# Performance work log

Measured on AMD Instinct MI355X. Metric: run time of the kernel, lower is better.

The kernel has to match this reference:

```python
import jax, jax.numpy as jnp
import numpy as np

B, C_IN, C_OUT, N, K = 4, 64, 64, 100000, 6
EPS = 1e-5  # BatchNorm2d default eps


def setup_inputs() -> dict:
    key = jax.random.key(0)
    k1, k2, k3, k4 = jax.random.split(key, 4)
    x = jax.random.normal(k1, (B, C_IN, N), jnp.float32)
    neigh = jax.random.randint(k2, (B, N, K), 0, N, jnp.int32)
    # bias-free 1x2 conv weights (center feature + neighbor-sum symmetric operator)
    W0 = jax.random.normal(k3, (C_OUT, C_IN, 2), jnp.float32) * (1.0 / np.sqrt(C_IN * 2))
    W1 = jax.random.normal(k4, (C_OUT, C_OUT, 2), jnp.float32) * (1.0 / np.sqrt(C_OUT * 2))
    gamma = jnp.ones((C_OUT,), jnp.float32)
    beta = jnp.zeros((C_OUT,), jnp.float32)
    return {"x": x, "neigh": neigh, "W0": W0, "W1": W1, "gamma": gamma, "beta": beta}


def _mesh_conv_point(x, neigh, W):
    # x: [B, C, N], neigh: [B, N, K] -> gather neighbor features [B, C, N, K]
    nb = jax.vmap(lambda xb, ib: xb[:, ib])(x, neigh)
    # symmetric operator stack: center feature and sum over neighbors -> [B, C, N, 2]
    G = jnp.stack([x, nb.sum(axis=-1)], axis=-1)
    # 1x2 conv (bias=False) as einsum -> [B, O, N]
    return jnp.einsum('bcns,ocs->bon', G, W)


def _batchnorm(h, gamma, beta):
    # training-mode batch stats over (batch, vertex) per channel
    mean = h.mean(axis=(0, 2), keepdims=True)
    var = h.var(axis=(0, 2), keepdims=True)
    return (h - mean) * jax.lax.rsqrt(var + EPS) * gamma[None, :, None] + beta[None, :, None]


def reference(x, neigh, W0, W1, gamma, beta):
    h = _mesh_conv_point(x, neigh, W0)
    x1 = h  # residual branch
    h = _batchnorm(jax.nn.relu(h), gamma, beta)
    h = _mesh_conv_point(h, neigh, W1)
    h = h + x1
    return jax.nn.relu(h)
```

## Files before the change

kernel.cpp:

```cpp
#include <hip/hip_runtime.h>
#include <hip/hip_bf16.h>

#define BB   4
#define NN   100000
#define TOT  (BB * NN)
#define KK   6
#define EPSV 1e-5f

using bf16   = __hip_bfloat16;
using ushort = unsigned short;
typedef __attribute__((ext_vector_type(8))) short  short8;
typedef __attribute__((ext_vector_type(4))) float  float4v;

union U4S8 { uint4 u; short8 s; };

__device__ __forceinline__ unsigned f2bu(float f) {
    union { bf16 h; ushort u; } c; c.h = __float2bfloat16(f); return c.u;
}
__device__ __forceinline__ unsigned pk(float a, float b) {
    return f2bu(a) | (f2bu(b) << 16);
}
__device__ __forceinline__ float blo(unsigned x) {
    union { unsigned u; float f; } c; c.u = x << 16; return c.f;
}
__device__ __forceinline__ float bhi(unsigned x) {
    union { unsigned u; float f; } c; c.u = x & 0xFFFF0000u; return c.f;
}
__device__ __forceinline__ unsigned relu2(unsigned x) {
    unsigned lo = (unsigned)(((int)(x << 16)) >> 31) & 0x0000FFFFu;
    unsigned hi = ((unsigned)(((int)x) >> 31)) << 16;
    return x & ~(lo | hi);
}
__device__ __forceinline__ int batch_base(int g) {
    return (g >= 3 * NN) ? 3 * NN : (g >= 2 * NN) ? 2 * NN : (g >= NN) ? NN : 0;
}

__global__ void wprep0_k(const float* __restrict__ W0, ushort* __restrict__ Wf0)
{
    int L = blockIdx.x * 256 + threadIdx.x;
    if (L < 8192) {
        int i = L & 7, lane = (L >> 3) & 63, r = L >> 9;
        int s = r & 1, t = r >> 1;
        int o = (t & 3) * 16 + (lane & 15);
        int c = s * 32 + (lane >> 4) * 8 + i;
        Wf0[L] = f2bu(W0[o * 128 + c * 2 + (t >> 2)]);
    }
}

__global__ __launch_bounds__(256) void xpose_k(const float* __restrict__ x,
                                               ushort* __restrict__ xT)
{
    __shared__ float tile[64][65];
    const int b  = blockIdx.y;
    const int n0 = blockIdx.x * 64;
    const int tx = threadIdx.x & 63;
    const int ty = threadIdx.x >> 6;
    const float* xb = x + (size_t)b * 64 * NN;
    const int n = n0 + tx;
#pragma unroll
    for (int cc = 0; cc < 64; cc += 4) {
        const int c = cc + ty;
        tile[tx][c] = (n < NN) ? xb[(size_t)c * NN + n] : 0.f;
    }
    __syncthreads();
#pragma unroll
    for (int rr = 0; rr < 64; rr += 4) {
        const int nl = rr + ty;
        const int n2 = n0 + nl;
        if (n2 < NN) xT[((size_t)b * NN + n2) * 64 + tx] = (ushort)f2bu(tile[nl][tx]);
    }
}

__global__ __launch_bounds__(256, 3) void gemm1_k(
    const ushort* __restrict__ xT, const ushort* __restrict__ Wf,
    ushort* __restrict__ Uu, ushort* __restrict__ Uv)
{
    const int wave = threadIdx.x >> 6;
    const int lane = threadIdx.x & 63;
    const int col  = lane & 15;
    const int quad = lane >> 4;

    short8 wf[8][2];
#pragma unroll
    for (int t = 0; t < 8; ++t)
#pragma unroll
        for (int s = 0; s < 2; ++s)
            wf[t][s] = *(const short8*)(Wf + ((t * 2 + s) * 64 + lane) * 8);

    const int wid = blockIdx.x * 4 + wave;
    for (int tile = wid; tile < 25000; tile += 2500) {
        const size_t g0 = (size_t)tile * 16;
        const ushort* ar = xT + (g0 + col) * 64 + quad * 8;
        short8 p0 = *(const short8*)(ar);
        short8 p1 = *(const short8*)(ar + 32);

        float4v acc[8];
#pragma unroll
        for (int t = 0; t < 8; ++t) acc[t] = (float4v){0.f, 0.f, 0.f, 0.f};
#pragma unroll
        for (int t = 0; t < 8; ++t)
            acc[t] = __builtin_amdgcn_mfma_f32_16x16x32_bf16(wf[t][0], p0, acc[t], 0, 0, 0);
#pragma unroll
        for (int t = 0; t < 8; ++t)
            acc[t] = __builtin_amdgcn_mfma_f32_16x16x32_bf16(wf[t][1], p1, acc[t], 0, 0, 0);

#pragma unroll
        for (int t = 0; t < 8; ++t) {
            uint2 d;
            d.x = pk(acc[t][0], acc[t][1]);
            d.y = pk(acc[t][2], acc[t][3]);
            ushort* base = (t < 4) ? Uu : Uv;
            *(uint2*)(base + (g0 + col) * 64 + (t & 3) * 16 + quad * 4) = d;
        }
    }
}

__global__ __launch_bounds__(256, 4) void gather1_k(
    const ushort* __restrict__ Uu, const ushort* __restrict__ Uv,
    const int* __restrict__ neigh, ushort* __restrict__ hT,
    float* __restrict__ stats)
{
    __shared__ float red[4][128];
    const int wave = threadIdx.x >> 6;
    const int lane = threadIdx.x & 63;
    const int q    = lane >> 4;
    const int cpos = lane & 15;
    const int g0   = (blockIdx.x * 4 + wave) * 64;

    float sA[4] = {0, 0, 0, 0}, sB[4] = {0, 0, 0, 0};

    for (int it = 0; it < 8; ++it) {
        const int gb = g0 + it * 8;
        int gp[2], gc[2], bo[2];
        gp[0] = gb + q;     gp[1] = gb + 4 + q;
        gc[0] = (gp[0] < TOT) ? gp[0] : (TOT - 1);
        gc[1] = (gp[1] < TOT) ? gp[1] : (TOT - 1);
        bo[0] = batch_base(gc[0]);
        bo[1] = batch_base(gc[1]);

        int idx[2][6];
#pragma unroll
        for (int i = 0; i < 2; ++i)
#pragma unroll
            for (int k = 0; k < 6; ++k)
                idx[i][k] = neigh[(size_t)gc[i] * 6 + k];

        uint2 uu[2], vv[2][6];
#pragma unroll
        for (int i = 0; i < 2; ++i)
            uu[i] = *(const uint2*)(Uu + (size_t)gc[i] * 64 + cpos * 4);
#pragma unroll
        for (int i = 0; i < 2; ++i)
#pragma unroll
            for (int k = 0; k < 6; ++k)
                vv[i][k] = *(const uint2*)(Uv + (size_t)(bo[i] + idx[i][k]) * 64 + cpos * 4);

#pragma unroll
        for (int i = 0; i < 2; ++i) {
            float h[4];
            h[0] = blo(uu[i].x); h[1] = bhi(uu[i].x);
            h[2] = blo(uu[i].y); h[3] = bhi(uu[i].y);
#pragma unroll
            for (int k = 0; k < 6; ++k) {
                h[0] += blo(vv[i][k].x); h[1] += bhi(vv[i][k].x);
                h[2] += blo(vv[i][k].y); h[3] += bhi(vv[i][k].y);
            }
            if (gp[i] < TOT) {
                uint2 st;
                st.x = pk(h[0], h[1]);
                st.y = pk(h[2], h[3]);
                *(uint2*)(hT + (size_t)gp[i] * 64 + cpos * 4) = st;
#pragma unroll
                for (int j = 0; j < 4; ++j) {
                    float rv = fmaxf(h[j], 0.f);
                    sA[j] += rv;
                    sB[j]  = fmaf(rv, rv, sB[j]);
                }
            }
        }
    }

#pragma unroll
    for (int d = 16; d < 64; d <<= 1)
#pragma unroll
        for (int j = 0; j < 4; ++j) {
            sA[j] += __shfl_xor(sA[j], d);
            sB[j] += __shfl_xor(sB[j], d);
        }
    if (q == 0) {
#pragma unroll
        for (int j = 0; j < 4; ++j) {
            red[wave][cpos * 4 + j]      = sA[j];
            red[wave][64 + cpos * 4 + j] = sB[j];
        }
    }
    __syncthreads();
    if (threadIdx.x < 128) {
        float v = red[0][threadIdx.x] + red[1][threadIdx.x]
                + red[2][threadIdx.x] + red[3][threadIdx.x];
        atomicAdd(&stats[threadIdx.x], v);
    }
}

__global__ void bnA_k(const float* __restrict__ stats, const float* __restrict__ gamma,
                      const float* __restrict__ beta, float* __restrict__ ab)
{
    const int o = threadIdx.x;
    if (o < 64) {
        const float inv = 1.f / (float)TOT;
        float mean = stats[o] * inv;
        float var  = stats[64 + o] * inv - mean * mean;
        float a    = gamma[o] * rsqrtf(var + EPSV);
        ab[o]      = a;
        ab[64 + o] = fmaf(-a, mean, beta[o]);
    }
}

__global__ __launch_bounds__(256) void bnB_k(
    const float* __restrict__ ab, const float* __restrict__ W1,
    ushort* __restrict__ Wf1, float* __restrict__ bias)
{
    if (blockIdx.x < 32) {
        int L = blockIdx.x * 256 + threadIdx.x;
        int i = L & 7, lane = (L >> 3) & 63, r = L >> 9;
        int s = r & 1, t = r >> 1;
        int o = (t & 3) * 16 + (lane & 15);
        int c = s * 32 + (lane >> 4) * 8 + i;
        Wf1[L] = f2bu(ab[c] * W1[o * 128 + c * 2 + (t >> 2)]);
    } else if (threadIdx.x < 128) {
        const int part = threadIdx.x >> 6, o = threadIdx.x & 63;
        float s = 0.f;
#pragma unroll
        for (int c = 0; c < 64; ++c)
            s = fmaf(ab[64 + c], W1[o * 128 + c * 2 + part], s);
        bias[threadIdx.x] = s;
    }
}

__global__ __launch_bounds__(256, 3) void gemm2_k(
    const ushort* __restrict__ hT, const ushort* __restrict__ Wf,
    const float* __restrict__ bias, ushort* __restrict__ Up,
    ushort* __restrict__ Uq)
{
    const int wave = threadIdx.x >> 6;
    const int lane = threadIdx.x & 63;
    const int col  = lane & 15;
    const int quad = lane >> 4;

    short8 wf[8][2];
#pragma unroll
    for (int t = 0; t < 8; ++t)
#pragma unroll
        for (int s = 0; s < 2; ++s)
            wf[t][s] = *(const short8*)(Wf + ((t * 2 + s) * 64 + lane) * 8);

    float4v binit[8];
#pragma unroll
    for (int t = 0; t < 8; ++t)
#pragma unroll
        for (int r = 0; r < 4; ++r)
            binit[t][r] = bias[t * 16 + quad * 4 + r];

    const int wid = blockIdx.x * 4 + wave;
    for (int tile = wid; tile < 25000; tile += 2500) {
        const size_t g0 = (size_t)tile * 16;
        const ushort* ar = hT + (g0 + col) * 64 + quad * 8;
        U4S8 p0, p1;
        p0.u = *(const uint4*)(ar);
        p1.u = *(const uint4*)(ar + 32);
        p0.u.x = relu2(p0.u.x); p0.u.y = relu2(p0.u.y);
        p0.u.z = relu2(p0.u.z); p0.u.w = relu2(p0.u.w);
        p1.u.x = relu2(p1.u.x); p1.u.y = relu2(p1.u.y);
        p1.u.z = relu2(p1.u.z); p1.u.w = relu2(p1.u.w);

        float4v acc[8];
#pragma unroll
        for (int t = 0; t < 8; ++t) acc[t] = binit[t];
#pragma unroll
        for (int t = 0; t < 8; ++t)
            acc[t] = __builtin_amdgcn_mfma_f32_16x16x32_bf16(wf[t][0], p0.s, acc[t], 0, 0, 0);
#pragma unroll
        for (int t = 0; t < 8; ++t)
            acc[t] = __builtin_amdgcn_mfma_f32_16x16x32_bf16(wf[t][1], p1.s, acc[t], 0, 0, 0);

#pragma unroll
        for (int t = 0; t < 8; ++t) {
            uint2 d;
            d.x = pk(acc[t][0], acc[t][1]);
            d.y = pk(acc[t][2], acc[t][3]);
            ushort* base = (t < 4) ? Up : Uq;
            *(uint2*)(base + (g0 + col) * 64 + (t & 3) * 16 + quad * 4) = d;
        }
    }
}

__global__ __launch_bounds__(256, 4) void gather2_k(
    const ushort* __restrict__ Up, const ushort* __restrict__ Uq,
    const ushort* __restrict__ hT, const int* __restrict__ neigh,
    float* __restrict__ out)
{
    __shared__ float ts[64][65];
    const int wave = threadIdx.x >> 6;
    const int lane = threadIdx.x & 63;
    const int q    = lane >> 4;
    const int cpos = lane & 15;
    const int g0   = blockIdx.x * 64;

#pragma unroll
    for (int it = 0; it < 2; ++it) {
        const int gb = g0 + wave * 16 + it * 8;
        int gp[2], bo[2];
        gp[0] = gb + q;  gp[1] = gb + 4 + q;
        bo[0] = batch_base(gp[0]);
        bo[1] = batch_base(gp[1]);

        int idx[2][6];
#pragma unroll
        for (int i = 0; i < 2; ++i)
#pragma unroll
            for (int k = 0; k < 6; ++k)
                idx[i][k] = neigh[(size_t)gp[i] * 6 + k];

        uint2 pp[2], rr[2], qq[2][6];
#pragma unroll
        for (int i = 0; i < 2; ++i) {
            pp[i] = *(const uint2*)(Up + (size_t)gp[i] * 64 + cpos * 4);
            rr[i] = *(const uint2*)(hT + (size_t)gp[i] * 64 + cpos * 4);
        }
#pragma unroll
        for (int i = 0; i < 2; ++i)
#pragma unroll
            for (int k = 0; k < 6; ++k)
                qq[i][k] = *(const uint2*)(Uq + (size_t)(bo[i] + idx[i][k]) * 64 + cpos * 4);

#pragma unroll
        for (int i = 0; i < 2; ++i) {
            float h[4];
            h[0] = blo(pp[i].x) + blo(rr[i].x); h[1] = bhi(pp[i].x) + bhi(rr[i].x);
            h[2] = blo(pp[i].y) + blo(rr[i].y); h[3] = bhi(pp[i].y) + bhi(rr[i].y);
#pragma unroll
            for (int k = 0; k < 6; ++k) {
                h[0] += blo(qq[i][k].x); h[1] += bhi(qq[i][k].x);
                h[2] += blo(qq[i][k].y); h[3] += bhi(qq[i][k].y);
            }
            const int pl = wave * 16 + it * 8 + i * 4 + q;
#pragma unroll
            for (int j = 0; j < 4; ++j)
                ts[cpos * 4 + j][pl] = fmaxf(h[j], 0.f);
        }
    }
    __syncthreads();

    const int g2  = g0 + lane;
    const int bo2 = batch_base(g2);
    const int b2  = (g2 >= 3 * NN) ? 3 : (g2 >= 2 * NN) ? 2 : (g2 >= NN) ? 1 : 0;
    const int n2  = g2 - bo2;
#pragma unroll
    for (int r = 0; r < 16; ++r) {
        const int o = wave * 16 + r;
        out[((size_t)b2 * 64 + o) * NN + n2] = ts[o][lane];
    }
}

extern "C" void kernel_launch(void* const* d_in, const int* in_sizes, int n_in,
                              void* d_out, int out_size, void* d_ws, size_t ws_size,
                              hipStream_t stream)
{
    const float* x     = (const float*)d_in[0];
    const int*   neigh = (const int*)d_in[1];
    const float* W0    = (const float*)d_in[2];
    const float* W1    = (const float*)d_in[3];
    const float* gamma = (const float*)d_in[4];
    const float* beta  = (const float*)d_in[5];
    float* out = (float*)d_out;

    char* ws = (char*)d_ws;
    ushort* xT    = (ushort*)(ws + 0);
    ushort* hT    = (ushort*)(ws + 0);
    ushort* Uu    = (ushort*)(ws + 51200000);
    ushort* Uv    = (ushort*)(ws + 102400000);
    ushort* Up    = Uu;
    ushort* Uq    = Uv;
    float*  stats = (float*)(ws + 153600000);
    float*  ab    = (float*)(ws + 153600512);
    ushort* Wf0   = (ushort*)(ws + 153601024);
    ushort* Wf1   = (ushort*)(ws + 153617408);
    float*  bias  = (float*)(ws + 153633792);

    hipMemsetAsync(stats, 0, 512, stream);
    wprep0_k<<<dim3(32), dim3(256), 0, stream>>>(W0, Wf0);
    xpose_k<<<dim3((NN + 63) / 64, BB), dim3(256), 0, stream>>>(x, xT);
    gemm1_k<<<dim3(625), dim3(256), 0, stream>>>(xT, Wf0, Uu, Uv);
    gather1_k<<<dim3(1563), dim3(256), 0, stream>>>(Uu, Uv, neigh, hT, stats);
    bnA_k<<<dim3(1), dim3(64), 0, stream>>>(stats, gamma, beta, ab);
    bnB_k<<<dim3(33), dim3(256), 0, stream>>>(ab, W1, Wf1, bias);
    gemm2_k<<<dim3(625), dim3(256), 0, stream>>>(hT, Wf1, bias, Up, Uq);
    gather2_k<<<dim3(TOT / 64), dim3(256), 0, stream>>>(Up, Uq, hT, neigh, out);
}
```

Measured before the change: 432.5 us.

## Stage neighbor gathers through LDS via global_load_lds with swizzled rows

Both gather kernels now fetch the six neighbor rows with 16-byte global_load_lds direct-to-LDS loads into a per-wave staging buffer, using a rotating swizzle so the LDS reads avoid bank conflicts. Each lane handles 8 channels with 16-byte loads and stores instead of 4 channels with 8-byte accesses, and neighbor indices are read as uint2 pairs. gather1 is relaunched with twice the blocks and fewer points per wave. The aim is wider, fewer memory transactions and less register pressure from in-flight gathers. In exchange it adds LDS use, lowers the occupancy hint to 3, and waits on vmcnt(0) every iteration, so loads from one iteration cannot overlap the next.

```diff
diff --git a/kernel.cpp b/kernel.cpp
--- a/kernel.cpp
+++ b/kernel.cpp
@@ -33,6 +33,13 @@
 }
 __device__ __forceinline__ int batch_base(int g) {
     return (g >= 3 * NN) ? 3 * NN : (g >= 2 * NN) ? 2 * NN : (g >= NN) ? NN : 0;
+}
+
+__device__ __forceinline__ void gload_lds16(const void* g, void* l)
+{
+    __builtin_amdgcn_global_load_lds(
+        (const __attribute__((address_space(1))) unsigned int*)g,
+        (__attribute__((address_space(3))) unsigned int*)l, 16, 0, 0);
 }
 
 __global__ void wprep0_k(const float* __restrict__ W0, ushort* __restrict__ Wf0)
@@ -115,83 +122,77 @@
     }
 }
 
-__global__ __launch_bounds__(256, 4) void gather1_k(
+__global__ __launch_bounds__(256, 3) void gather1_k(
     const ushort* __restrict__ Uu, const ushort* __restrict__ Uv,
     const int* __restrict__ neigh, ushort* __restrict__ hT,
     float* __restrict__ stats)
 {
+    __shared__ __align__(1024) ushort stage[4][3072];
     __shared__ float red[4][128];
     const int wave = threadIdx.x >> 6;
     const int lane = threadIdx.x & 63;
-    const int q    = lane >> 4;
-    const int cpos = lane & 15;
-    const int g0   = (blockIdx.x * 4 + wave) * 64;
-
-    float sA[4] = {0, 0, 0, 0}, sB[4] = {0, 0, 0, 0};
-
-    for (int it = 0; it < 8; ++it) {
-        const int gb = g0 + it * 8;
-        int gp[2], gc[2], bo[2];
-        gp[0] = gb + q;     gp[1] = gb + 4 + q;
-        gc[0] = (gp[0] < TOT) ? gp[0] : (TOT - 1);
-        gc[1] = (gp[1] < TOT) ? gp[1] : (TOT - 1);
-        bo[0] = batch_base(gc[0]);
-        bo[1] = batch_base(gc[1]);
-
-        int idx[2][6];
-#pragma unroll
-        for (int i = 0; i < 2; ++i)
-#pragma unroll
-            for (int k = 0; k < 6; ++k)
-                idx[i][k] = neigh[(size_t)gc[i] * 6 + k];
-
-        uint2 uu[2], vv[2][6];
-#pragma unroll
-        for (int i = 0; i < 2; ++i)
-            uu[i] = *(const uint2*)(Uu + (size_t)gc[i] * 64 + cpos * 4);
-#pragma unroll
-        for (int i = 0; i < 2; ++i)
-#pragma unroll
-            for (int k = 0; k < 6; ++k)
-                vv[i][k] = *(const uint2*)(Uv + (size_t)(bo[i] + idx[i][k]) * 64 + cpos * 4);
-
-#pragma unroll
-        for (int i = 0; i < 2; ++i) {
-            float h[4];
-            h[0] = blo(uu[i].x); h[1] = bhi(uu[i].x);
-            h[2] = blo(uu[i].y); h[3] = bhi(uu[i].y);
-#pragma unroll
-            for (int k = 0; k < 6; ++k) {
-                h[0] += blo(vv[i][k].x); h[1] += bhi(vv[i][k].x);
-                h[2] += blo(vv[i][k].y); h[3] += bhi(vv[i][k].y);
-            }
-            if (gp[i] < TOT) {
-                uint2 st;
-                st.x = pk(h[0], h[1]);
-                st.y = pk(h[2], h[3]);
-                *(uint2*)(hT + (size_t)gp[i] * 64 + cpos * 4) = st;
-#pragma unroll
-                for (int j = 0; j < 4; ++j) {
-                    float rv = fmaxf(h[j], 0.f);
-                    sA[j] += rv;
-                    sB[j]  = fmaf(rv, rv, sB[j]);
-                }
-            }
-        }
-    }
-
-#pragma unroll
-    for (int d = 16; d < 64; d <<= 1)
-#pragma unroll
-        for (int j = 0; j < 4; ++j) {
+    const int p    = lane >> 3;
+    const int s    = lane & 7;
+    const int g0   = (blockIdx.x * 4 + wave) * 32;
+
+    ushort* stg = stage[wave];
+    const int csw = ((s - p) & 7) * 8;
+    const int rsw = ((s + p) & 7) * 8;
+    const uint2* nbp = (const uint2*)neigh;
+
+    float sA[8] = {0,0,0,0,0,0,0,0}, sB[8] = {0,0,0,0,0,0,0,0};
+
+    for (int t = 0; t < 4; ++t) {
+        const int gme = g0 + t * 8 + p;
+        const int bo  = batch_base(gme);
+
+        uint2 i01 = nbp[(size_t)gme * 3 + 0];
+        uint2 i23 = nbp[(size_t)gme * 3 + 1];
+        uint2 i45 = nbp[(size_t)gme * 3 + 2];
+        int idx[6] = {(int)i01.x, (int)i01.y, (int)i23.x,
+                      (int)i23.y, (int)i45.x, (int)i45.y};
+
+        uint4 cu = *(const uint4*)(Uu + (size_t)gme * 64 + s * 8);
+
+#pragma unroll
+        for (int m = 0; m < 6; ++m)
+            gload_lds16(Uv + (size_t)(bo + idx[m]) * 64 + csw, stg + m * 512);
+
+        asm volatile("s_waitcnt vmcnt(0)" ::: "memory");
+
+        float h[8];
+        h[0] = blo(cu.x); h[1] = bhi(cu.x); h[2] = blo(cu.y); h[3] = bhi(cu.y);
+        h[4] = blo(cu.z); h[5] = bhi(cu.z); h[6] = blo(cu.w); h[7] = bhi(cu.w);
+#pragma unroll
+        for (int m = 0; m < 6; ++m) {
+            const uint4 r = *(const uint4*)(stg + m * 512 + p * 64 + rsw);
+            h[0] += blo(r.x); h[1] += bhi(r.x); h[2] += blo(r.y); h[3] += bhi(r.y);
+            h[4] += blo(r.z); h[5] += bhi(r.z); h[6] += blo(r.w); h[7] += bhi(r.w);
+        }
+        uint4 st;
+        st.x = pk(h[0], h[1]); st.y = pk(h[2], h[3]);
+        st.z = pk(h[4], h[5]); st.w = pk(h[6], h[7]);
+        *(uint4*)(hT + (size_t)gme * 64 + s * 8) = st;
+#pragma unroll
+        for (int j = 0; j < 8; ++j) {
+            float rv = fmaxf(h[j], 0.f);
+            sA[j] += rv;
+            sB[j]  = fmaf(rv, rv, sB[j]);
+        }
+    }
+
+#pragma unroll
+    for (int d = 8; d < 64; d <<= 1)
+#pragma unroll
+        for (int j = 0; j < 8; ++j) {
             sA[j] += __shfl_xor(sA[j], d);
             sB[j] += __shfl_xor(sB[j], d);
         }
-    if (q == 0) {
-#pragma unroll
-        for (int j = 0; j < 4; ++j) {
-            red[wave][cpos * 4 + j]      = sA[j];
-            red[wave][64 + cpos * 4 + j] = sB[j];
+    if (lane < 8) {
+#pragma unroll
+        for (int j = 0; j < 8; ++j) {
+            red[wave][lane * 8 + j]      = sA[j];
+            red[wave][64 + lane * 8 + j] = sB[j];
         }
     }
     __syncthreads();
@@ -294,60 +295,60 @@
     }
 }
 
-__global__ __launch_bounds__(256, 4) void gather2_k(
+__global__ __launch_bounds__(256, 3) void gather2_k(
     const ushort* __restrict__ Up, const ushort* __restrict__ Uq,
     const ushort* __restrict__ hT, const int* __restrict__ neigh,
     float* __restrict__ out)
 {
+    __shared__ __align__(1024) ushort stage[4][3072];
     __shared__ float ts[64][65];
     const int wave = threadIdx.x >> 6;
     const int lane = threadIdx.x & 63;
-    const int q    = lane >> 4;
-    const int cpos = lane & 15;
+    const int p    = lane >> 3;
+    const int s    = lane & 7;
     const int g0   = blockIdx.x * 64;
-
-#pragma unroll
-    for (int it = 0; it < 2; ++it) {
-        const int gb = g0 + wave * 16 + it * 8;
-        int gp[2], bo[2];
-        gp[0] = gb + q;  gp[1] = gb + 4 + q;
-        bo[0] = batch_base(gp[0]);
-        bo[1] = batch_base(gp[1]);
-
-        int idx[2][6];
-#pragma unroll
-        for (int i = 0; i < 2; ++i)
-#pragma unroll
-            for (int k = 0; k < 6; ++k)
-                idx[i][k] = neigh[(size_t)gp[i] * 6 + k];
-
-        uint2 pp[2], rr[2], qq[2][6];
-#pragma unroll
-        for (int i = 0; i < 2; ++i) {
-            pp[i] = *(const uint2*)(Up + (size_t)gp[i] * 64 + cpos * 4);
-            rr[i] = *(const uint2*)(hT + (size_t)gp[i] * 64 + cpos * 4);
-        }
-#pragma unroll
-        for (int i = 0; i < 2; ++i)
-#pragma unroll
-            for (int k = 0; k < 6; ++k)
-                qq[i][k] = *(const uint2*)(Uq + (size_t)(bo[i] + idx[i][k]) * 64 + cpos * 4);
-
-#pragma unroll
-        for (int i = 0; i < 2; ++i) {
-            float h[4];
-            h[0] = blo(pp[i].x) + blo(rr[i].x); h[1] = bhi(pp[i].x) + bhi(rr[i].x);
-            h[2] = blo(pp[i].y) + blo(rr[i].y); h[3] = bhi(pp[i].y) + bhi(rr[i].y);
-#pragma unroll
-            for (int k = 0; k < 6; ++k) {
-                h[0] += blo(qq[i][k].x); h[1] += bhi(qq[i][k].x);
-                h[2] += blo(qq[i][k].y); h[3] += bhi(qq[i][k].y);
-            }
-            const int pl = wave * 16 + it * 8 + i * 4 + q;
-#pragma unroll
-            for (int j = 0; j < 4; ++j)
-                ts[cpos * 4 + j][pl] = fmaxf(h[j], 0.f);
-        }
+    const int gw   = g0 + wave * 16;
+
+    ushort* stg = stage[wave];
+    const int csw = ((s - p) & 7) * 8;
+    const int rsw = ((s + p) & 7) * 8;
+    const uint2* nbp = (const uint2*)neigh;
+
+#pragma unroll
+    for (int t = 0; t < 2; ++t) {
+        const int gme = gw + t * 8 + p;
+        const int bo  = batch_base(gme);
+
+        uint2 i01 = nbp[(size_t)gme * 3 + 0];
+        uint2 i23 = nbp[(size_t)gme * 3 + 1];
+        uint2 i45 = nbp[(size_t)gme * 3 + 2];
+        int idx[6] = {(int)i01.x, (int)i01.y, (int)i23.x,
+                      (int)i23.y, (int)i45.x, (int)i45.y};
+
+        uint4 cp = *(const uint4*)(Up + (size_t)gme * 64 + s * 8);
+        uint4 cr = *(const uint4*)(hT + (size_t)gme * 64 + s * 8);
+
+#pragma unroll
+        for (int m = 0; m < 6; ++m)
+            gload_lds16(Uq + (size_t)(bo + idx[m]) * 64 + csw, stg + m * 512);
+
+        asm volatile("s_waitcnt vmcnt(0)" ::: "memory");
+
+        float h[8];
+        h[0] = blo(cp.x) + blo(cr.x); h[1] = bhi(cp.x) + bhi(cr.x);
+        h[2] = blo(cp.y) + blo(cr.y); h[3] = bhi(cp.y) + bhi(cr.y);
+        h[4] = blo(cp.z) + blo(cr.z); h[5] = bhi(cp.z) + bhi(cr.z);
+        h[6] = blo(cp.w) + blo(cr.w); h[7] = bhi(cp.w) + bhi(cr.w);
+#pragma unroll
+        for (int m = 0; m < 6; ++m) {
+            const uint4 r = *(const uint4*)(stg + m * 512 + p * 64 + rsw);
+            h[0] += blo(r.x); h[1] += bhi(r.x); h[2] += blo(r.y); h[3] += bhi(r.y);
+            h[4] += blo(r.z); h[5] += bhi(r.z); h[6] += blo(r.w); h[7] += bhi(r.w);
+        }
+        const int pl = wave * 16 + t * 8 + p;
+#pragma unroll
+        for (int j = 0; j < 8; ++j)
+            ts[s * 8 + j][pl] = fmaxf(h[j], 0.f);
     }
     __syncthreads();
 
@@ -391,7 +392,7 @@
     wprep0_k<<<dim3(32), dim3(256), 0, stream>>>(W0, Wf0);
     xpose_k<<<dim3((NN + 63) / 64, BB), dim3(256), 0, stream>>>(x, xT);
     gemm1_k<<<dim3(625), dim3(256), 0, stream>>>(xT, Wf0, Uu, Uv);
-    gather1_k<<<dim3(1563), dim3(256), 0, stream>>>(Uu, Uv, neigh, hT, stats);
+    gather1_k<<<dim3(3125), dim3(256), 0, stream>>>(Uu, Uv, neigh, hT, stats);
     bnA_k<<<dim3(1), dim3(64), 0, stream>>>(stats, gamma, beta, ab);
     bnB_k<<<dim3(33), dim3(256), 0, stream>>>(ab, W1, Wf1, bias);
     gemm2_k<<<dim3(625), dim3(256), 0, stream>>>(hT, Wf1, bias, Up, Uq);
```

Measured after the change: 442.9 us. 2.4% more time.
